# Performance work log

Measured on AMD Instinct MI355X. Metric: run time of the kernel, lower is better.

The kernel has to match this reference:

```python
import jax, jax.numpy as jnp
import numpy as np

# Module config (matches init_kwargs)
K_W, K_H = 3, 3
C_IN, C_OUT = 64, 64
B, W_IN, H_IN = 8, 32, 32
J = K_W * K_H * C_IN  # flattened patch length, torch layout (c_in, k_w, k_h)


def setup_inputs() -> dict:
    key = jax.random.key(0)
    k_x, k_w = jax.random.split(key)
    x = jax.random.normal(k_x, (B, W_IN, H_IN, C_IN), dtype=jnp.float32)
    # reset_parameters: randint{0,1} * 2 - 1 -> weights in {-1, +1}
    weights = jax.random.randint(k_w, (C_OUT, J), 0, 2).astype(jnp.float32) * 2.0 - 1.0
    return {"input": x, "weights": weights}


def reference(input, weights):
    b, w_in, h_in, c_in = input.shape
    pw, ph = K_W // 2, K_H // 2
    # F.pad(..., value=-1) pads the two spatial dims, channels untouched
    xp = jnp.pad(input, ((0, 0), (pw, pw), (ph, ph), (0, 0)), constant_values=-1.0)
    # torch .unfold(1,k_w,1).unfold(2,k_h,1) -> (B, W, H, c_in, k_w, k_h)
    patches = jnp.stack(
        [jnp.stack([xp[:, u:u + w_in, v:v + h_in, :] for v in range(K_H)], axis=-1)
         for u in range(K_W)],
        axis=-2,
    )  # (B, W, H, c_in, k_w, k_h)
    # flatten patch, then view flat axis as (k_w, k_h*c_in) exactly like the
    # torch reshape([-1, k_w, k_h*c_in]) (a pure regrouping of the flat axis)
    u = patches.reshape(b * w_in * h_in, K_W, K_H * c_in)  # (N, k_w, k_h*c_in)
    wv = weights.reshape(C_OUT, K_W, K_H * c_in)            # (A, k_w, k_h*c_in)
    # einsum('bj,aj->baj') then sum over the k_w-sized chunk axis == contract u
    inter = jnp.einsum('nug,aug->nag', u, wv)               # (N, c_out, k_h*c_in)
    # majority vote: clamp to [-1,1], scale by 3, reduce
    out = jnp.sum(jnp.clip(inter, -1.0, 1.0) * 3.0, axis=-1)  # (N, c_out)
    return out.reshape(b, w_in, h_in, C_OUT)
```

## Files before the change

### kernel.cpp

```cpp
#include <hip/hip_runtime.h>


#define TW 2240

typedef float f4 __attribute__((ext_vector_type(4)));

__device__ __forceinline__ float clip1(float s) {
    return __builtin_amdgcn_fmed3f(s, -1.0f, 1.0f);
}

template <int T0>
__device__ __forceinline__ void g_half(const float* __restrict__ tile,
                                       const float* __restrict__ w,
                                       int a0u, int Bb, float acc[4]) {
    int Bw = Bb;
#pragma unroll 1
    for (int ci = 0; ci < 10; ++ci) {
        float xv[3][3][3];
#pragma unroll
        for (int k = 0; k < 3; ++k)
#pragma unroll
            for (int U = 0; U < 3; ++U) {
                const int u   = (T0 + k + 64 * U) % 3;
                const int Kc  = (T0 + k + 64 * U - u) / 3;
                const int off = u * TW + Kc * 35;
#pragma unroll
                for (int d = 0; d < 3; ++d)
                    xv[k][U][d] = tile[Bw + off + d];
            }
#pragma unroll
        for (int ch = 0; ch < 4; ++ch) {
            const float* wp = w + (a0u + ch) * 576 + 3 * T0 + 9 * ci;
            float wf[3][9];
#pragma unroll
            for (int U = 0; U < 3; ++U)
#pragma unroll
                for (int q = 0; q < 9; ++q) wf[U][q] = wp[U * 192 + q];
            float a = acc[ch];
#pragma unroll
            for (int k = 0; k < 3; ++k)
#pragma unroll
                for (int d = 0; d < 3; ++d) {
                    float s = fmaf(xv[k][0][d], wf[0][3 * k + d],
                              fmaf(xv[k][1][d], wf[1][3 * k + d],
                                   xv[k][2][d] * wf[2][3 * k + d]));
                    a += clip1(s);
                }
            acc[ch] = a;
        }
        Bw += 35;
    }
    {
        float xv[2][3][3];
#pragma unroll
        for (int k = 0; k < 2; ++k)
#pragma unroll
            for (int U = 0; U < 3; ++U) {
                const int u   = (T0 + k + 64 * U) % 3;
                const int Kc  = (T0 + k + 64 * U - u) / 3;
                const int off = u * TW + Kc * 35;
#pragma unroll
                for (int d = 0; d < 3; ++d)
                    xv[k][U][d] = tile[Bw + off + d];
            }
#pragma unroll
        for (int ch = 0; ch < 4; ++ch) {
            const float* wp = w + (a0u + ch) * 576 + 3 * T0 + 90;
            float wf[3][6];
#pragma unroll
            for (int U = 0; U < 3; ++U)
#pragma unroll
                for (int q = 0; q < 6; ++q) wf[U][q] = wp[U * 192 + q];
            float a = acc[ch];
#pragma unroll
            for (int k = 0; k < 2; ++k)
#pragma unroll
                for (int d = 0; d < 3; ++d) {
                    float s = fmaf(xv[k][0][d], wf[0][3 * k + d],
                              fmaf(xv[k][1][d], wf[1][3 * k + d],
                                   xv[k][2][d] * wf[2][3 * k + d]));
                    a += clip1(s);
                }
            acc[ch] = a;
        }
    }
}

__global__ __launch_bounds__(256, 4) void maj3_kernel(
        const float* __restrict__ x, const float* __restrict__ w,
        float* __restrict__ out) {
    __shared__ float tile[4 * TW];
    __shared__ float red[2][4][64];

    const int tid  = threadIdx.x;
    const int lane = tid & 63;
    const int wid  = tid >> 6;
    const int blk  = blockIdx.x;
    const int set  = blk >> 3;
    const int a0b  = (blk & 7) << 3;
    const int bimg = set >> 4;
    const int w0   = (set & 15) << 1;

    {
        const int wx  = w0 + wid - 1;
        const bool ok = (unsigned)wx < 32u;
        const float* xp = x + ((bimg * 32 + wx) * 32) * 64 + lane;
        float vs[34];
#pragma unroll
        for (int hh = 0; hh < 34; ++hh) {
            const int hx = hh - 1;
            vs[hh] = -1.0f;
            if (ok && (unsigned)hx < 32u) vs[hh] = xp[hx * 64];
        }
#pragma unroll
        for (int hh = 0; hh < 34; ++hh)
            tile[wid * TW + lane * 35 + hh] = vs[hh];
    }
    __syncthreads();

    const int chgrp = (wid >> 1) & 1;
    const int ghalf = wid & 1;
    const int a0u   = __builtin_amdgcn_readfirstlane(a0b + chgrp * 4);
    const int Bb    = (lane >> 5) * TW + (lane & 31);

    float acc[4] = {0.f, 0.f, 0.f, 0.f};
    if (ghalf == 0) g_half<0>(tile, w, a0u, Bb, acc);
    else            g_half<32>(tile, w, a0u, Bb, acc);

    if (ghalf == 1) {
#pragma unroll
        for (int k = 0; k < 4; ++k) red[chgrp][k][lane] = acc[k];
    }
    __syncthreads();

    if (ghalf == 0) {
        const int wl = lane >> 5, hl = lane & 31;
        float* op = out + ((bimg * 32 + w0 + wl) * 32 + hl) * 64 + a0u;
        f4 o;
#pragma unroll
        for (int k = 0; k < 4; ++k)
            o[k] = 3.0f * (acc[k] + red[chgrp][k][lane]);
        *(f4*)op = o;
    }
}

extern "C" void kernel_launch(void* const* d_in, const int* in_sizes, int n_in,
                              void* d_out, int out_size, void* d_ws, size_t ws_size,
                              hipStream_t stream) {
    const float* x = (const float*)d_in[0];
    const float* w = (const float*)d_in[1];
    float* out = (float*)d_out;
    maj3_kernel<<<1024, 256, 0, stream>>>(x, w, out);
}
```

Measured before the change: 72.74 us.

## Split patch contraction into quarters per wave with 8 channels each

Changes the per-wave work split: instead of two channel groups × two halves of the contraction, each of the four waves now handles a quarter of the group axis for all 8 output channels of the block. Each loaded set of input values from shared memory is therefore reused across 8 channels instead of 4, cutting LDS traffic per FLOP. The three partial sums are reduced through the reused tile buffer, which needs an extra barrier. Register pressure rises with 8 accumulators and the larger unrolled weight loads, and only one wave does the final stores.

```diff
diff --git a/kernel.cpp b/kernel.cpp
--- a/kernel.cpp
+++ b/kernel.cpp
@@ -10,12 +10,12 @@
 }
 
 template <int T0>
-__device__ __forceinline__ void g_half(const float* __restrict__ tile,
-                                       const float* __restrict__ w,
-                                       int a0u, int Bb, float acc[4]) {
+__device__ __forceinline__ void g_quarter(const float* __restrict__ tile,
+                                          const float* __restrict__ w,
+                                          int a0, int Bb, float acc[8]) {
     int Bw = Bb;
 #pragma unroll 1
-    for (int ci = 0; ci < 10; ++ci) {
+    for (int ci = 0; ci < 5; ++ci) {
         float xv[3][3][3];
 #pragma unroll
         for (int k = 0; k < 3; ++k)
@@ -29,8 +29,8 @@
                     xv[k][U][d] = tile[Bw + off + d];
             }
 #pragma unroll
-        for (int ch = 0; ch < 4; ++ch) {
-            const float* wp = w + (a0u + ch) * 576 + 3 * T0 + 9 * ci;
+        for (int ch = 0; ch < 8; ++ch) {
+            const float* wp = w + (a0 + ch) * 576 + 3 * T0 + 9 * ci;
             float wf[3][9];
 #pragma unroll
             for (int U = 0; U < 3; ++U)
@@ -51,36 +51,32 @@
         Bw += 35;
     }
     {
-        float xv[2][3][3];
+        float xv[3][3];
 #pragma unroll
-        for (int k = 0; k < 2; ++k)
+        for (int U = 0; U < 3; ++U) {
+            const int u   = (T0 + 64 * U) % 3;
+            const int Kc  = (T0 + 64 * U - u) / 3;
+            const int off = u * TW + Kc * 35;
 #pragma unroll
-            for (int U = 0; U < 3; ++U) {
-                const int u   = (T0 + k + 64 * U) % 3;
-                const int Kc  = (T0 + k + 64 * U - u) / 3;
-                const int off = u * TW + Kc * 35;
+            for (int d = 0; d < 3; ++d)
+                xv[U][d] = tile[Bw + off + d];
+        }
 #pragma unroll
-                for (int d = 0; d < 3; ++d)
-                    xv[k][U][d] = tile[Bw + off + d];
-            }
-#pragma unroll
-        for (int ch = 0; ch < 4; ++ch) {
-            const float* wp = w + (a0u + ch) * 576 + 3 * T0 + 90;
-            float wf[3][6];
+        for (int ch = 0; ch < 8; ++ch) {
+            const float* wp = w + (a0 + ch) * 576 + 3 * T0 + 45;
+            float wf[3][3];
 #pragma unroll
             for (int U = 0; U < 3; ++U)
 #pragma unroll
-                for (int q = 0; q < 6; ++q) wf[U][q] = wp[U * 192 + q];
+                for (int q = 0; q < 3; ++q) wf[U][q] = wp[U * 192 + q];
             float a = acc[ch];
 #pragma unroll
-            for (int k = 0; k < 2; ++k)
-#pragma unroll
-                for (int d = 0; d < 3; ++d) {
-                    float s = fmaf(xv[k][0][d], wf[0][3 * k + d],
-                              fmaf(xv[k][1][d], wf[1][3 * k + d],
-                                   xv[k][2][d] * wf[2][3 * k + d]));
-                    a += clip1(s);
-                }
+            for (int d = 0; d < 3; ++d) {
+                float s = fmaf(xv[0][d], wf[0][d],
+                          fmaf(xv[1][d], wf[1][d],
+                               xv[2][d] * wf[2][d]));
+                a += clip1(s);
+            }
             acc[ch] = a;
         }
     }
@@ -90,14 +86,13 @@
         const float* __restrict__ x, const float* __restrict__ w,
         float* __restrict__ out) {
     __shared__ float tile[4 * TW];
-    __shared__ float red[2][4][64];
 
     const int tid  = threadIdx.x;
     const int lane = tid & 63;
     const int wid  = tid >> 6;
     const int blk  = blockIdx.x;
     const int set  = blk >> 3;
-    const int a0b  = (blk & 7) << 3;
+    const int a0   = (blk & 7) << 3;
     const int bimg = set >> 4;
     const int w0   = (set & 15) << 1;
 
@@ -118,29 +113,36 @@
     }
     __syncthreads();
 
-    const int chgrp = (wid >> 1) & 1;
-    const int ghalf = wid & 1;
-    const int a0u   = __builtin_amdgcn_readfirstlane(a0b + chgrp * 4);
-    const int Bb    = (lane >> 5) * TW + (lane & 31);
+    const int Bb = (lane >> 5) * TW + (lane & 31);
 
-    float acc[4] = {0.f, 0.f, 0.f, 0.f};
-    if (ghalf == 0) g_half<0>(tile, w, a0u, Bb, acc);
-    else            g_half<32>(tile, w, a0u, Bb, acc);
+    float acc[8] = {0, 0, 0, 0, 0, 0, 0, 0};
+    if      (wid == 0) g_quarter<0>(tile, w, a0, Bb, acc);
+    else if (wid == 1) g_quarter<16>(tile, w, a0, Bb, acc);
+    else if (wid == 2) g_quarter<32>(tile, w, a0, Bb, acc);
+    else               g_quarter<48>(tile, w, a0, Bb, acc);
 
-    if (ghalf == 1) {
+    __syncthreads();
+    if (wid != 0) {
 #pragma unroll
-        for (int k = 0; k < 4; ++k) red[chgrp][k][lane] = acc[k];
+        for (int k = 0; k < 8; ++k)
+            tile[((wid - 1) * 8 + k) * 64 + lane] = acc[k];
     }
     __syncthreads();
 
-    if (ghalf == 0) {
+    if (wid == 0) {
         const int wl = lane >> 5, hl = lane & 31;
-        float* op = out + ((bimg * 32 + w0 + wl) * 32 + hl) * 64 + a0u;
-        f4 o;
+        float* op = out + ((bimg * 32 + w0 + wl) * 32 + hl) * 64 + a0;
+        f4 o0, o1;
 #pragma unroll
-        for (int k = 0; k < 4; ++k)
-            o[k] = 3.0f * (acc[k] + red[chgrp][k][lane]);
-        *(f4*)op = o;
+        for (int k = 0; k < 8; ++k) {
+            float v = acc[k] + tile[(0 * 8 + k) * 64 + lane]
+                             + tile[(1 * 8 + k) * 64 + lane]
+                             + tile[(2 * 8 + k) * 64 + lane];
+            if (k < 4) o0[k] = 3.0f * v;
+            else       o1[k - 4] = 3.0f * v;
+        }
+        *(f4*)(op)     = o0;
+        *(f4*)(op + 4) = o1;
     }
 }
 
```

New measurement: 72.60 us. About the same (-0.2%).
